# Optimization experiments

Measured on AMD Instinct MI355X. Metric: run time of the kernel, lower is better.

The kernel has to match this reference:

```python
import jax, jax.numpy as jnp
import numpy as np
from jax import lax

FILTER_DIM = 11  # FIR taps
BATCH = 128
N = 262144  # samples per frame
CHANNELS = 1
STRIDES = 1


def setup_inputs() -> dict:
    key = jax.random.key(0)
    kx, kp = jax.random.split(key)
    X = jax.random.normal(kx, (BATCH, N, 2), dtype=jnp.float32)
    # learned FIR filter: (filter_dim, 2, channels) -> [:,0,:]=real taps, [:,1,:]=imag taps
    phi = jax.random.normal(kp, (FILTER_DIM, 2, CHANNELS), dtype=jnp.float32)
    return {"X": X, "phi": phi}


def _conv1d(x, w):
    # x: (B, N, 1), w: (K, 1, 1); TF-style SAME cross-correlation, channels_last
    return lax.conv_general_dilated(
        x, w, window_strides=(STRIDES,), padding="SAME",
        dimension_numbers=("NWC", "WIO", "NWC"))


def reference(X, phi):
    # X: (B, N, 2) complex as [real, imag]; phi: (K, 2, 1)
    X_real = X[:, :, 0:1]            # (B, N, 1)
    X_img = X[:, :, 1:2]             # (B, N, 1)
    phi_real = phi[:, 0, :][:, None, :]  # (K, 1, 1)
    phi_img = phi[:, 1, :][:, None, :]   # (K, 1, 1)
    # complex convolution: (Xr + i Xi) * (pr + i pi)
    real = _conv1d(X_real, phi_real) - _conv1d(X_img, phi_img)  # (B, N, 1)
    img = _conv1d(X_real, phi_img) + _conv1d(X_img, phi_real)   # (B, N, 1)
    return jnp.concatenate([real, img], axis=2)  # (B, N, 2)
```

## Files before the change

### kernel.cpp

```cpp
#include <hip/hip_runtime.h>


constexpr int N_SAMP  = 262144;
constexpr int BATCH   = 128;
constexpr int TAPS    = 11;
constexpr int HALO    = 5;
constexpr int BLOCK   = 256;
constexpr int VEC     = 4;
constexpr int TILE    = BLOCK * VEC;
constexpr int SMEM_N  = TILE + 2 * HALO;

__global__ __launch_bounds__(BLOCK)
void fir_complex_kernel(const float2* __restrict__ X,
                        const float*  __restrict__ phi,
                        float2*       __restrict__ out)
{
    __shared__ float2 s[SMEM_N];

    const int tile_idx   = blockIdx.x;
    const int b          = blockIdx.y;
    const int t          = threadIdx.x;
    const int tile_start = tile_idx * TILE;
    const long long row  = (long long)b * N_SAMP;

    float pr[TAPS], pi[TAPS];
#pragma unroll
    for (int k = 0; k < TAPS; ++k) {
        pr[k] = phi[2 * k + 0];
        pi[k] = phi[2 * k + 1];
    }

    const int g0 = tile_start - HALO;
#pragma unroll
    for (int r = 0; r < (SMEM_N + BLOCK - 1) / BLOCK; ++r) {
        const int i = r * BLOCK + t;
        if (i < SMEM_N) {
            const int n = g0 + i;
            float2 v = make_float2(0.0f, 0.0f);
            if ((unsigned)n < (unsigned)N_SAMP) v = X[row + n];
            s[i] = v;
        }
    }
    __syncthreads();

#pragma unroll
    for (int j = 0; j < VEC; ++j) {
        const int l = t + j * BLOCK;
        float re = 0.0f, im = 0.0f;
#pragma unroll
        for (int k = 0; k < TAPS; ++k) {
            const float2 v = s[l + k];
            re = fmaf(v.x, pr[k], re);
            re = fmaf(-v.y, pi[k], re);
            im = fmaf(v.x, pi[k], im);
            im = fmaf(v.y, pr[k], im);
        }
        out[row + tile_start + l] = make_float2(re, im);
    }
}

extern "C" void kernel_launch(void* const* d_in, const int* in_sizes, int n_in,
                              void* d_out, int out_size, void* d_ws, size_t ws_size,
                              hipStream_t stream)
{
    const float2* X   = (const float2*)d_in[0];
    const float*  phi = (const float*)d_in[1];
    float2*       out = (float2*)d_out;

    dim3 grid(N_SAMP / TILE, BATCH);
    fir_complex_kernel<<<grid, BLOCK, 0, stream>>>(X, phi, out);
}
```

Measured before the change: 422.1 us.

## Replace shared-memory tiling with per-thread register windows and float4 I/O

Each thread now loads a contiguous 20-sample window straight from global memory into registers using float4 loads. It computes 8 consecutive outputs from that window and writes them back with float4 stores. This removes the LDS staging and the block barrier. The cost is redundant halo reads for each thread (20 loads for 8 outputs), which rely on the cache. Per-thread strided vector accesses may also coalesce worse than the old consecutive-thread pattern.

```diff
diff --git a/kernel.cpp b/kernel.cpp
--- a/kernel.cpp
+++ b/kernel.cpp
@@ -1,27 +1,24 @@
 #include <hip/hip_runtime.h>
 
 
-constexpr int N_SAMP  = 262144;
-constexpr int BATCH   = 128;
-constexpr int TAPS    = 11;
-constexpr int HALO    = 5;
-constexpr int BLOCK   = 256;
-constexpr int VEC     = 4;
-constexpr int TILE    = BLOCK * VEC;
-constexpr int SMEM_N  = TILE + 2 * HALO;
+constexpr int N_SAMP = 262144;
+constexpr int BATCH  = 128;
+constexpr int TAPS   = 11;
+constexpr int BLOCK  = 256;
+constexpr int VEC    = 8;
+constexpr int TILE   = BLOCK * VEC;
+constexpr int NW     = VEC + 12;
 
 __global__ __launch_bounds__(BLOCK)
 void fir_complex_kernel(const float2* __restrict__ X,
                         const float*  __restrict__ phi,
                         float2*       __restrict__ out)
 {
-    __shared__ float2 s[SMEM_N];
-
-    const int tile_idx   = blockIdx.x;
-    const int b          = blockIdx.y;
-    const int t          = threadIdx.x;
-    const int tile_start = tile_idx * TILE;
-    const long long row  = (long long)b * N_SAMP;
+    const int  t    = threadIdx.x;
+    const int  b    = blockIdx.y;
+    const long long row = (long long)b * N_SAMP;
+    const int  c    = blockIdx.x * TILE + t * VEC;
+    const int  w0   = c - 6;
 
     float pr[TAPS], pi[TAPS];
 #pragma unroll
@@ -30,32 +27,45 @@
         pi[k] = phi[2 * k + 1];
     }
 
-    const int g0 = tile_start - HALO;
+    float2 w[NW];
+    const bool interior = (w0 >= 0) && (w0 + NW <= N_SAMP);
+    if (interior) {
+        const float4* p = (const float4*)(X + row + w0);
 #pragma unroll
-    for (int r = 0; r < (SMEM_N + BLOCK - 1) / BLOCK; ++r) {
-        const int i = r * BLOCK + t;
-        if (i < SMEM_N) {
-            const int n = g0 + i;
-            float2 v = make_float2(0.0f, 0.0f);
-            if ((unsigned)n < (unsigned)N_SAMP) v = X[row + n];
-            s[i] = v;
+        for (int i = 0; i < NW / 2; ++i) {
+            const float4 v = p[i];
+            w[2 * i + 0] = make_float2(v.x, v.y);
+            w[2 * i + 1] = make_float2(v.z, v.w);
+        }
+    } else {
+#pragma unroll
+        for (int i = 0; i < NW; ++i) {
+            const int n = w0 + i;
+            w[i] = ((unsigned)n < (unsigned)N_SAMP) ? X[row + n]
+                                                    : make_float2(0.0f, 0.0f);
         }
     }
-    __syncthreads();
 
+    float2 acc[VEC];
 #pragma unroll
     for (int j = 0; j < VEC; ++j) {
-        const int l = t + j * BLOCK;
         float re = 0.0f, im = 0.0f;
 #pragma unroll
         for (int k = 0; k < TAPS; ++k) {
-            const float2 v = s[l + k];
-            re = fmaf(v.x, pr[k], re);
+            const float2 v = w[j + k + 1];
+            re = fmaf(v.x,  pr[k], re);
             re = fmaf(-v.y, pi[k], re);
-            im = fmaf(v.x, pi[k], im);
-            im = fmaf(v.y, pr[k], im);
+            im = fmaf(v.x,  pi[k], im);
+            im = fmaf(v.y,  pr[k], im);
         }
-        out[row + tile_start + l] = make_float2(re, im);
+        acc[j] = make_float2(re, im);
+    }
+
+    float4* po = (float4*)(out + row + c);
+#pragma unroll
+    for (int i = 0; i < VEC / 2; ++i) {
+        po[i] = make_float4(acc[2 * i].x, acc[2 * i].y,
+                            acc[2 * i + 1].x, acc[2 * i + 1].y);
     }
 }
 
```

Result: slower. 448.2 us (+6.2%).
